# Kernel tuning notes

Measured on AMD Instinct MI355X. Metric: run time of the kernel, lower is better.

Reference implementation:

```python
import jax, jax.numpy as jnp
import numpy as np

N = 512
D = 128        # d_model
DE = 128       # d_edge
DFF = 2048
H = 8          # n_head
DH = D // H
LN_EPS = 1e-5


def layer_norm(x, g, b):
    m = jnp.mean(x, axis=-1, keepdims=True)
    v = jnp.mean((x - m) ** 2, axis=-1, keepdims=True)
    return (x - m) * jax.lax.rsqrt(v + LN_EPS) * g + b


def setup_inputs() -> dict:
    key = jax.random.key(0)
    ks = jax.random.split(key, 20)
    s = 0.02
    d = {
        "node": jax.random.normal(ks[0], (N, D), jnp.float32),
        "edge": jax.random.normal(ks[1], (N, N, DE), jnp.float32),
        "edge_mask": jnp.zeros((N, N), dtype=bool),
        # proj_memory: Linear(d_edge+2*d_model -> d_model) split by concat blocks [edge|src|tar]
        "w_mem_e": s * jax.random.normal(ks[2], (DE, D), jnp.float32),
        "w_mem_s": s * jax.random.normal(ks[3], (D, D), jnp.float32),
        "w_mem_t": s * jax.random.normal(ks[4], (D, D), jnp.float32),
        "b_mem": jnp.zeros((D,), jnp.float32),
        "g_ln_mem": jnp.ones((D,), jnp.float32),
        "b_ln_mem": jnp.zeros((D,), jnp.float32),
        # proj_edge: Linear(d_model -> d_edge) + LN, then norm_edge
        "w_pe": s * jax.random.normal(ks[5], (D, DE), jnp.float32),
        "b_pe": jnp.zeros((DE,), jnp.float32),
        "g_ln_pe": jnp.ones((DE,), jnp.float32),
        "b_ln_pe": jnp.zeros((DE,), jnp.float32),
        "g_ln_edge": jnp.ones((DE,), jnp.float32),
        "b_ln_edge": jnp.zeros((DE,), jnp.float32),
        # MHA in/out projections
        "wq": s * jax.random.normal(ks[6], (D, D), jnp.float32),
        "bq": jnp.zeros((D,), jnp.float32),
        "wk": s * jax.random.normal(ks[7], (D, D), jnp.float32),
        "bk": jnp.zeros((D,), jnp.float32),
        "wv": s * jax.random.normal(ks[8], (D, D), jnp.float32),
        "bv": jnp.zeros((D,), jnp.float32),
        "wo": s * jax.random.normal(ks[9], (D, D), jnp.float32),
        "bo": jnp.zeros((D,), jnp.float32),
        "g_ln2": jnp.ones((D,), jnp.float32),
        "b_ln2": jnp.zeros((D,), jnp.float32),
        # FFN
        "w_ff1": s * jax.random.normal(ks[10], (D, DFF), jnp.float32),
        "b_ff1": jnp.zeros((DFF,), jnp.float32),
        "w_ff2": s * jax.random.normal(ks[11], (DFF, D), jnp.float32),
        "b_ff2": jnp.zeros((D,), jnp.float32),
        "g_ln3": jnp.ones((D,), jnp.float32),
        "b_ln3": jnp.zeros((D,), jnp.float32),
    }
    return d


def reference(node, edge, edge_mask,
              w_mem_e, w_mem_s, w_mem_t, b_mem, g_ln_mem, b_ln_mem,
              w_pe, b_pe, g_ln_pe, b_ln_pe, g_ln_edge, b_ln_edge,
              wq, bq, wk, bk, wv, bv, wo, bo, g_ln2, b_ln2,
              w_ff1, b_ff1, w_ff2, b_ff2, g_ln3, b_ln3):
    # ---- _build_memory ----
    # torch concat order [edge, src_x, tar_x]: src_x[i,j]=node[j], tar_x[i,j]=node[i].
    # Avoid materializing the (N,N,2D+DE) concat: split the linear by block.
    mem_pre = (jnp.einsum('ijd,df->ijf', edge, w_mem_e)
               + (node @ w_mem_s)[None, :, :]
               + (node @ w_mem_t)[:, None, :]
               + b_mem)                                   # (N, N, D)
    memory = jax.nn.relu(layer_norm(mem_pre, g_ln_mem, b_ln_mem))
    edge_upd = jax.nn.relu(layer_norm(memory @ w_pe + b_pe, g_ln_pe, b_ln_pe))
    edge_new = layer_norm(edge + edge_upd, g_ln_edge, b_ln_edge)  # (N, N, DE)

    # ---- MHA: query len 1, batch N, key/value = memory (src_len=N, batch=N) ----
    q = (node @ wq + bq).reshape(N, H, DH)                # (Nb, H, DH)
    k = (jnp.einsum('snd,df->snf', memory, wk) + bk).reshape(N, N, H, DH)  # (S, Nb, H, DH)
    v = (jnp.einsum('snd,df->snf', memory, wv) + bv).reshape(N, N, H, DH)
    scores = jnp.einsum('nhd,snhd->nhs', q, k) / jnp.sqrt(jnp.float32(DH))  # (Nb, H, S)
    scores = jnp.where(edge_mask[:, None, :], jnp.finfo(scores.dtype).min, scores)
    attn = jax.nn.softmax(scores, axis=-1)
    ctx = jnp.einsum('nhs,snhd->nhd', attn, v).reshape(N, D)
    x_prime = ctx @ wo + bo                               # (N, D)

    # ---- residual + norms + FFN ----
    x = layer_norm(node + x_prime, g_ln2, b_ln2)
    ff = jax.nn.relu(x @ w_ff1 + b_ff1) @ w_ff2 + b_ff2
    x = layer_norm(x + ff, g_ln3, b_ln3)
    return (x, edge_new)
```

## Files before the change

### kernel.cpp

```cpp
#include <hip/hip_runtime.h>

#define NN 512
#define DD 128
#define DFF 2048
#define HH 8
#define DHH 16

typedef __attribute__((ext_vector_type(8))) short short8;
typedef __attribute__((ext_vector_type(4))) float f32x4;

static __device__ __forceinline__ float bf2f(ushort u) {
    union { unsigned int i; float f; } v; v.i = ((unsigned int)u) << 16; return v.f;
}
static __device__ __forceinline__ ushort f2bf(float f) {
    union { float f; unsigned int i; } v; v.f = f;
    unsigned int x = v.i;
    return (ushort)((x + 0x7fffu + ((x >> 16) & 1u)) >> 16);
}
static __device__ __forceinline__ short8 pack8(float4 v0, float4 v1) {
    short8 u;
    u[0]=(short)f2bf(v0.x); u[1]=(short)f2bf(v0.y);
    u[2]=(short)f2bf(v0.z); u[3]=(short)f2bf(v0.w);
    u[4]=(short)f2bf(v1.x); u[5]=(short)f2bf(v1.y);
    u[6]=(short)f2bf(v1.z); u[7]=(short)f2bf(v1.w);
    return u;
}

static __device__ __forceinline__ int probe_f32(const void* p) {
    return (((const ushort*)p)[0] == 0) ? 1 : 0;
}
static __device__ __forceinline__ float ld(const void* p, size_t i, int f32) {
    return f32 ? ((const float*)p)[i] : bf2f(((const ushort*)p)[i]);
}
static __device__ __forceinline__ void st(void* p, size_t i, float v, int f32) {
    if (f32) ((float*)p)[i] = v; else ((ushort*)p)[i] = f2bf(v);
}

static __device__ __forceinline__ ushort* mem_row_ptr(void* out_base, void* wsmem,
                                                      int big, int f32, int r) {
    if (big) return (ushort*)wsmem + (size_t)r * DD;
    char* b = (char*)out_base;
    return f32 ? (ushort*)(b + (size_t)4*NN*DD + (size_t)r*4*DD)
               : (ushort*)(b + (size_t)2*NN*DD + (size_t)r*2*DD);
}

static __device__ __forceinline__ int swz(int row, int b) {
    return row*256 + (b ^ ((row & 15) << 4));
}

static __device__ __forceinline__ float2 ln_tree(float v, float* red, float* red2) {
    const int t = threadIdx.x;
    __syncthreads();
    red[t] = v; red2[t] = v * v;
    __syncthreads();
    for (int s = 64; s > 0; s >>= 1) {
        if (t < s) { red[t] += red[t + s]; red2[t] += red2[t + s]; }
        __syncthreads();
    }
    float mean = red[0] * (1.f / 128.f);
    float var  = red2[0] * (1.f / 128.f) - mean * mean;
    float2 r; r.x = mean; r.y = rsqrtf(fmaxf(var, 0.f) + 1e-5f);
    return r;
}

__global__ __launch_bounds__(256) void k_wconv(
    const void* __restrict__ w_mem_e, const void* __restrict__ w_pe,
    const void* __restrict__ dt_probe, ushort* __restrict__ wf)
{
    const int f32 = probe_f32(dt_probe);
    int idx = blockIdx.x * 256 + threadIdx.x;
    const void* W = (idx < 32768) ? w_mem_e : w_pe;
    int rem = idx & 32767;
    int b = rem & 7, lane = (rem >> 3) & 63, ks = (rem >> 9) & 3, tn = rem >> 11;
    int k = ks*32 + (lane >> 4)*8 + b;
    int n = tn*16 + (lane & 15);
    wf[idx] = f2bf(ld(W, (size_t)k*DD + n, f32));
}

__global__ __launch_bounds__(256) void k_wconv2(
    const void* __restrict__ w_ff1, const void* __restrict__ w_ff2,
    const void* __restrict__ dt_probe, ushort* __restrict__ wf)
{
    const int f32 = probe_f32(dt_probe);
    int idx = blockIdx.x * 256 + threadIdx.x;
    if (idx < 262144) {
        int b = idx & 7, lane = (idx >> 3) & 63, ks = (idx >> 9) & 3, ct = idx >> 11;
        int k = ks*32 + (lane >> 4)*8 + b;
        int n = ct*16 + (lane & 15);
        wf[idx] = f2bf(ld(w_ff1, (size_t)k*DFF + n, f32));
    } else {
        int rem = idx - 262144;
        int b = rem & 7, lane = (rem >> 3) & 63, kc = (rem >> 9) & 63, tn = rem >> 15;
        int k = kc*32 + (lane >> 4)*8 + b;
        int n = tn*16 + (lane & 15);
        wf[idx] = f2bf(ld(w_ff2, (size_t)k*DD + n, f32));
    }
}

__global__ __launch_bounds__(128) void k_pre(
    const void* __restrict__ node, const void* __restrict__ w_mem_s,
    const void* __restrict__ w_mem_t, const void* __restrict__ wq,
    const void* __restrict__ bq, const void* __restrict__ wk,
    const void* __restrict__ bk, const void* __restrict__ dt_probe,
    float* __restrict__ a_s, float* __restrict__ a_t,
    float* __restrict__ qw, float* __restrict__ qb)
{
    const int f32 = probe_f32(dt_probe);
    const int n = blockIdx.x;
    const int t = threadIdx.x;
    __shared__ float nr[DD];
    __shared__ float qr[DD];
    nr[t] = ld(node, (size_t)n*DD + t, f32);
    __syncthreads();
    float s_acc = 0.f, t_acc = 0.f, q_acc = ld(bq, t, f32);
    for (int k = 0; k < DD; ++k) {
        float nv = nr[k];
        s_acc += nv * ld(w_mem_s, (size_t)k*DD + t, f32);
        t_acc += nv * ld(w_mem_t, (size_t)k*DD + t, f32);
        q_acc += nv * ld(wq,      (size_t)k*DD + t, f32);
    }
    a_s[(size_t)n*DD + t] = s_acc;
    a_t[(size_t)n*DD + t] = t_acc;
    qr[t] = q_acc;
    __syncthreads();
    for (int h = 0; h < HH; ++h) {
        float acc = 0.f;
        #pragma unroll
        for (int dh = 0; dh < DHH; ++dh)
            acc += qr[h*DHH + dh] * ld(wk, (size_t)t*DD + h*DHH + dh, f32);
        qw[((size_t)n*HH + h)*DD + t] = acc;
    }
    if (t < HH) {
        float acc = 0.f;
        #pragma unroll
        for (int dh = 0; dh < DHH; ++dh)
            acc += qr[t*DHH + dh] * ld(bk, (size_t)t*DHH + dh, f32);
        qb[(size_t)n*HH + t] = acc;
    }
}

__global__ __launch_bounds__(256) void k_fused(
    const void* __restrict__ edge, const ushort* __restrict__ wfe,
    const ushort* __restrict__ wfp, const void* __restrict__ b_mem,
    const void* __restrict__ g1, const void* __restrict__ b1,
    const void* __restrict__ b_pe, const void* __restrict__ g2,
    const void* __restrict__ b2, const void* __restrict__ g3,
    const void* __restrict__ b3, const void* __restrict__ dt_probe,
    const float* __restrict__ a_s, const float* __restrict__ a_t,
    void* __restrict__ out_base, ushort* __restrict__ memws)
{
    const int f32 = probe_f32(dt_probe);
    const int t = threadIdx.x;
    const int r0 = blockIdx.x * 64;
    const int i0 = r0 >> 9;
    const int j0 = r0 & (NN - 1);

    __shared__ __align__(16) ushort tile[64*128];

    const int lane = t & 63, w = t >> 6;
    const int rowbase = w * 16;
    const int l15 = lane & 15, g = lane >> 4;
    const int arow = r0 + rowbase + l15;

    short8 afr[4];
    if (f32) {
        const float* ep = (const float*)edge + (size_t)arow*DD;
        #pragma unroll
        for (int ks = 0; ks < 4; ++ks) {
            float4 v0 = *(const float4*)(ep + ks*32 + g*8);
            float4 v1 = *(const float4*)(ep + ks*32 + g*8 + 4);
            afr[ks] = pack8(v0, v1);
        }
    } else {
        const ushort* ep = (const ushort*)edge + (size_t)arow*DD;
        #pragma unroll
        for (int ks = 0; ks < 4; ++ks)
            afr[ks] = *(const short8*)(ep + ks*32 + g*8);
    }

    f32x4 acc[8];
    #pragma unroll
    for (int tn = 0; tn < 8; ++tn) {
        acc[tn][0]=0.f; acc[tn][1]=0.f; acc[tn][2]=0.f; acc[tn][3]=0.f;
    }
    #pragma unroll
    for (int tn = 0; tn < 8; ++tn) {
        #pragma unroll
        for (int ks = 0; ks < 4; ++ks) {
            short8 bfr = *(const short8*)(wfe + ((tn*4 + ks)*64 + lane)*8);
            acc[tn] = __builtin_amdgcn_mfma_f32_16x16x32_bf16(afr[ks], bfr,
                                                              acc[tn], 0, 0, 0);
        }
    }

    float atb[8], gg[8], bb[8];
    #pragma unroll
    for (int tn = 0; tn < 8; ++tn) {
        int c = tn*16 + l15;
        atb[tn] = a_t[(size_t)i0*DD + c] + ld(b_mem, c, f32);
        gg[tn]  = ld(g1, c, f32);
        bb[tn]  = ld(b1, c, f32);
    }

    float sum[4], sq[4];
    #pragma unroll
    for (int reg = 0; reg < 4; ++reg) {
        const int rr = rowbase + 4*g + reg;
        float s = 0.f, qq = 0.f;
        #pragma unroll
        for (int tn = 0; tn < 8; ++tn) {
            float v = acc[tn][reg]
                    + a_s[(size_t)(j0 + rr)*DD + tn*16 + l15] + atb[tn];
            acc[tn][reg] = v;
            s += v; qq += v*v;
        }
        sum[reg] = s; sq[reg] = qq;
    }
    #pragma unroll
    for (int m = 1; m < 16; m <<= 1) {
        #pragma unroll
        for (int reg = 0; reg < 4; ++reg) {
            sum[reg] += __shfl_xor(sum[reg], m, 64);
            sq[reg]  += __shfl_xor(sq[reg],  m, 64);
        }
    }
    #pragma unroll
    for (int reg = 0; reg < 4; ++reg) {
        const int rr = rowbase + 4*g + reg;
        float mean = sum[reg] * (1.f/128.f);
        float var  = sq[reg] * (1.f/128.f) - mean*mean;
        float rstd = rsqrtf(fmaxf(var, 0.f) + 1e-5f);
        #pragma unroll
        for (int tn = 0; tn < 8; ++tn) {
            float v = fmaxf((acc[tn][reg]-mean)*rstd*gg[tn] + bb[tn], 0.f);
            *(ushort*)((char*)tile + swz(rr, (tn*16 + l15)*2)) = f2bf(v);
        }
    }

    {
        const int crow = rowbase + l15;
        ushort* dst = memws + (size_t)(r0 + crow)*DD;
        #pragma unroll
        for (int q = 0; q < 4; ++q)
            *(short8*)(dst + g*32 + q*8) =
                *(const short8*)((const char*)tile + swz(crow, g*64 + q*16));
    }

    short8 afr2[4];
    #pragma unroll
    for (int ks = 0; ks < 4; ++ks)
        afr2[ks] = *(const short8*)((const char*)tile
                    + swz(rowbase + l15, ks*64 + g*16));

    f32x4 acc2[8];
    #pragma unroll
    for (int tn = 0; tn < 8; ++tn) {
        acc2[tn][0]=0.f; acc2[tn][1]=0.f; acc2[tn][2]=0.f; acc2[tn][3]=0.f;
    }
    #pragma unroll
    for (int tn = 0; tn < 8; ++tn) {
        #pragma unroll
        for (int ks = 0; ks < 4; ++ks) {
            short8 bfr = *(const short8*)(wfp + ((tn*4 + ks)*64 + lane)*8);
            acc2[tn] = __builtin_amdgcn_mfma_f32_16x16x32_bf16(afr2[ks], bfr,
                                                               acc2[tn], 0, 0, 0);
        }
    }

    float bpe[8], gg2[8], bb2[8], gg3v[8], bb3v[8];
    #pragma unroll
    for (int tn = 0; tn < 8; ++tn) {
        int c = tn*16 + l15;
        bpe[tn]  = ld(b_pe, c, f32);
        gg2[tn]  = ld(g2, c, f32); bb2[tn] = ld(b2, c, f32);
        gg3v[tn] = ld(g3, c, f32); bb3v[tn] = ld(b3, c, f32);
    }

    float s1[4], q1[4];
    #pragma unroll
    for (int reg = 0; reg < 4; ++reg) {
        float s = 0.f, qq = 0.f;
        #pragma unroll
        for (int tn = 0; tn < 8; ++tn) {
            float v = acc2[tn][reg] + bpe[tn];
            acc2[tn][reg] = v;
            s += v; qq += v*v;
        }
        s1[reg] = s; q1[reg] = qq;
    }
    #pragma unroll
    for (int m = 1; m < 16; m <<= 1) {
        #pragma unroll
        for (int reg = 0; reg < 4; ++reg) {
            s1[reg] += __shfl_xor(s1[reg], m, 64);
            q1[reg] += __shfl_xor(q1[reg], m, 64);
        }
    }

    float s2[4], q2[4];
    #pragma unroll
    for (int reg = 0; reg < 4; ++reg) {
        const int rr = rowbase + 4*g + reg;
        float mean = s1[reg] * (1.f/128.f);
        float var  = q1[reg] * (1.f/128.f) - mean*mean;
        float rstd = rsqrtf(fmaxf(var, 0.f) + 1e-5f);
        float ss = 0.f, qq = 0.f;
        #pragma unroll
        for (int tn = 0; tn < 8; ++tn) {
            float upd = fmaxf((acc2[tn][reg]-mean)*rstd*gg2[tn] + bb2[tn], 0.f);
            float ev  = ld(edge, (size_t)(r0 + rr)*DD + tn*16 + l15, f32);
            float y = ev + upd;
            acc2[tn][reg] = y;
            ss += y; qq += y*y;
        }
        s2[reg] = ss; q2[reg] = qq;
    }
    #pragma unroll
    for (int m = 1; m < 16; m <<= 1) {
        #pragma unroll
        for (int reg = 0; reg < 4; ++reg) {
            s2[reg] += __shfl_xor(s2[reg], m, 64);
            q2[reg] += __shfl_xor(q2[reg], m, 64);
        }
    }
    #pragma unroll
    for (int reg = 0; reg < 4; ++reg) {
        const int rr = rowbase + 4*g + reg;
        float mean = s2[reg] * (1.f/128.f);
        float var  = q2[reg] * (1.f/128.f) - mean*mean;
        float rstd = rsqrtf(fmaxf(var, 0.f) + 1e-5f);
        #pragma unroll
        for (int tn = 0; tn < 8; ++tn) {
            float outv = (acc2[tn][reg]-mean)*rstd*gg3v[tn] + bb3v[tn];
            st(out_base, (size_t)NN*DD + (size_t)(r0 + rr)*DD + tn*16 + l15,
               outv, f32);
        }
    }
}

__global__ __launch_bounds__(256) void k_mem_mfma(
    const void* __restrict__ edge, const ushort* __restrict__ wfe,
    const void* __restrict__ b_mem, const void* __restrict__ g1,
    const void* __restrict__ b1, const void* __restrict__ dt_probe,
    const float* __restrict__ a_s, const float* __restrict__ a_t,
    void* __restrict__ out_base, void* __restrict__ wsmem, int big)
{
    const int f32 = probe_f32(dt_probe);
    const int t = threadIdx.x;
    const int r0 = blockIdx.x * 64;
    const int i0 = r0 >> 9;
    const int j0 = r0 & (NN - 1);

    __shared__ __align__(16) ushort tile[64*128];

    {
        const int row = t >> 2;
        const int c0  = (t & 3) * 32;
        if (f32) {
            const float4* gp = (const float4*)((const float*)edge
                               + (size_t)(r0 + row)*DD + c0);
            #pragma unroll
            for (int q = 0; q < 4; ++q)
                *(short8*)((char*)tile + swz(row, c0*2 + q*16)) =
                    pack8(gp[2*q], gp[2*q+1]);
        } else {
            const short8* gp = (const short8*)((const ushort*)edge
                               + (size_t)(r0 + row)*DD + c0);
            #pragma unroll
            for (int q = 0; q < 4; ++q)
                *(short8*)((char*)tile + swz(row, c0*2 + q*16)) = gp[q];
        }
    }
    __syncthreads();

    const int lane = t & 63, w = t >> 6;
    const int rowbase = w * 16;
    const int l15 = lane & 15, g = lane >> 4;

    short8 afr[4];
    #pragma unroll
    for (int ks = 0; ks < 4; ++ks)
        afr[ks] = *(const short8*)((const char*)tile
                   + swz(rowbase + l15, ks*64 + g*16));

    f32x4 acc[8];
    #pragma unroll
    for (int tn = 0; tn < 8; ++tn) {
        acc[tn][0]=0.f; acc[tn][1]=0.f; acc[tn][2]=0.f; acc[tn][3]=0.f;
    }
    #pragma unroll
    for (int tn = 0; tn < 8; ++tn) {
        #pragma unroll
        for (int ks = 0; ks < 4; ++ks) {
            short8 bfr = *(const short8*)(wfe + ((tn*4 + ks)*64 + lane)*8);
            acc[tn] = __builtin_amdgcn_mfma_f32_16x16x32_bf16(afr[ks], bfr,
                                                              acc[tn], 0, 0, 0);
        }
    }

    float atb[8], gg[8], bb[8];
    #pragma unroll
    for (int tn = 0; tn < 8; ++tn) {
        int c = tn*16 + l15;
        atb[tn] = a_t[(size_t)i0*DD + c] + ld(b_mem, c, f32);
        gg[tn]  = ld(g1, c, f32);
        bb[tn]  = ld(b1, c, f32);
    }

    float sum[4], sq[4];
    #pragma unroll
    for (int reg = 0; reg < 4; ++reg) {
        const int rr = rowbase + 4*g + reg;
        float s = 0.f, qq = 0.f;
        #pragma unroll
        for (int tn = 0; tn < 8; ++tn) {
            float v = acc[tn][reg]
                    + a_s[(size_t)(j0 + rr)*DD + tn*16 + l15] + atb[tn];
            acc[tn][reg] = v;
            s += v; qq += v*v;
        }
        sum[reg] = s; sq[reg] = qq;
    }
    #pragma unroll
    for (int m = 1; m < 16; m <<= 1) {
        #pragma unroll
        for (int reg = 0; reg < 4; ++reg) {
            sum[reg] += __shfl_xor(sum[reg], m, 64);
            sq[reg]  += __shfl_xor(sq[reg],  m, 64);
        }
    }
    #pragma unroll
    for (int reg = 0; reg < 4; ++reg) {
        const int rr = rowbase + 4*g + reg;
        float mean = sum[reg] * (1.f/128.f);
        float var  = sq[reg] * (1.f/128.f) - mean*mean;
        float rstd = rsqrtf(fmaxf(var, 0.f) + 1e-5f);
        #pragma unroll
        for (int tn = 0; tn < 8; ++tn) {
            float v = fmaxf((acc[tn][reg]-mean)*rstd*gg[tn] + bb[tn], 0.f);
            *(ushort*)((char*)tile + swz(rr, (tn*16 + l15)*2)) = f2bf(v);
        }
    }
    __syncthreads();

    {
        const int crow = rowbase + l15;
        ushort* dst = mem_row_ptr(out_base, wsmem, big, f32, r0 + crow);
        #pragma unroll
        for (int q = 0; q < 4; ++q)
            *(short8*)(dst + g*32 + q*8) =
                *(const short8*)((const char*)tile + swz(crow, g*64 + q*16));
    }
}

__global__ __launch_bounds__(256) void k_attn(
    const float* __restrict__ qw, const float* __restrict__ qb,
    const unsigned char* __restrict__ mask,
    const void* __restrict__ wv_w, const void* __restrict__ bv,
    const void* __restrict__ dt_probe,
    void* __restrict__ out_base, void* __restrict__ wsmem, int big,
    float* __restrict__ ctx)
{
    const int f32 = probe_f32(dt_probe);
    const int n = blockIdx.x;
    const int t = threadIdx.x;

    __shared__ __align__(16) float qwl[HH*DD];
    __shared__ float qbl[HH];
    __shared__ __align__(16) float sc[HH*NN];
    __shared__ __align__(16) float msub[64*132];
    __shared__ float srd[HH*33];
    __shared__ __align__(16) float pml[HH*DD];

    #pragma unroll
    for (int u = 0; u < 4; ++u) qwl[t + 256*u] = qw[(size_t)n*HH*DD + t + 256*u];
    if (t < HH) qbl[t] = qb[(size_t)n*HH + t];
    __syncthreads();

    const int h0 = t >> 6;
    const int sl = t & 63;

    for (int s0 = 0; s0 < NN; s0 += 64) {
        __syncthreads();
        #pragma unroll
        for (int u = 0; u < 4; ++u) {
            int c = u*256 + t;
            int row = c >> 4, sub = c & 15;
            const ushort* src = mem_row_ptr(out_base, wsmem, big, f32,
                                            (s0 + row)*NN + n) + sub*8;
            short8 uv = *(const short8*)src;
            float4 x0, x1;
            x0.x=bf2f((ushort)uv[0]); x0.y=bf2f((ushort)uv[1]);
            x0.z=bf2f((ushort)uv[2]); x0.w=bf2f((ushort)uv[3]);
            x1.x=bf2f((ushort)uv[4]); x1.y=bf2f((ushort)uv[5]);
            x1.z=bf2f((ushort)uv[6]); x1.w=bf2f((ushort)uv[7]);
            float* d = msub + row*132 + sub*8;
            *(float4*)d = x0; *(float4*)(d + 4) = x1;
        }
        __syncthreads();
        float a0 = 0.f, a1 = 0.f;
        const float* mrow = msub + sl*132;
        const float* q0p = qwl + h0*DD;
        const float* q1p = qwl + (h0+4)*DD;
        for (int d = 0; d < DD; d += 4) {
            float4 mv = *(const float4*)(mrow + d);
            float4 qa = *(const float4*)(q0p + d);
            float4 qc = *(const float4*)(q1p + d);
            a0 += mv.x*qa.x + mv.y*qa.y + mv.z*qa.z + mv.w*qa.w;
            a1 += mv.x*qc.x + mv.y*qc.y + mv.z*qc.z + mv.w*qc.w;
        }
        int s = s0 + sl;
        int mk = mask[(size_t)n*NN + s] != 0;
        sc[h0*NN + s]     = mk ? -1.0e30f : 0.25f*(a0 + qbl[h0]);
        sc[(h0+4)*NN + s] = mk ? -1.0e30f : 0.25f*(a1 + qbl[h0+4]);
    }
    __syncthreads();

    {
        const int h = t >> 5, l = t & 31;
        float mx = -1.0e30f;
        for (int k = 0; k < 16; ++k) mx = fmaxf(mx, sc[h*NN + l + 32*k]);
        srd[h*33 + l] = mx;
        __syncthreads();
        for (int s = 16; s > 0; s >>= 1) {
            if (l < s) srd[h*33 + l] = fmaxf(srd[h*33 + l], srd[h*33 + l + s]);
            __syncthreads();
        }
        mx = srd[h*33];
        __syncthreads();
        float sum = 0.f;
        for (int k = 0; k < 16; ++k) {
            float e = __expf(sc[h*NN + l + 32*k] - mx);
            sc[h*NN + l + 32*k] = e;
            sum += e;
        }
        srd[h*33 + l] = sum;
        __syncthreads();
        for (int s = 16; s > 0; s >>= 1) {
            if (l < s) srd[h*33 + l] += srd[h*33 + l + s];
            __syncthreads();
        }
        float inv = 1.f / srd[h*33];
        for (int k = 0; k < 16; ++k) sc[h*NN + l + 32*k] *= inv;
    }
    __syncthreads();

    const int h2 = t >> 5, d4 = (t & 31) * 4;
    float4 acc2; acc2.x = 0.f; acc2.y = 0.f; acc2.z = 0.f; acc2.w = 0.f;
    for (int s0 = 0; s0 < NN; s0 += 64) {
        __syncthreads();
        #pragma unroll
        for (int u = 0; u < 4; ++u) {
            int c = u*256 + t;
            int row = c >> 4, sub = c & 15;
            const ushort* src = mem_row_ptr(out_base, wsmem, big, f32,
                                            (s0 + row)*NN + n) + sub*8;
            short8 uv = *(const short8*)src;
            float4 x0, x1;
            x0.x=bf2f((ushort)uv[0]); x0.y=bf2f((ushort)uv[1]);
            x0.z=bf2f((ushort)uv[2]); x0.w=bf2f((ushort)uv[3]);
            x1.x=bf2f((ushort)uv[4]); x1.y=bf2f((ushort)uv[5]);
            x1.z=bf2f((ushort)uv[6]); x1.w=bf2f((ushort)uv[7]);
            float* d = msub + row*132 + sub*8;
            *(float4*)d = x0; *(float4*)(d + 4) = x1;
        }
        __syncthreads();
        for (int s = 0; s < 64; ++s) {
            float wgt = sc[h2*NN + s0 + s];
            float4 mv = *(const float4*)(msub + s*132 + d4);
            acc2.x += wgt*mv.x; acc2.y += wgt*mv.y;
            acc2.z += wgt*mv.z; acc2.w += wgt*mv.w;
        }
    }
    *(float4*)(pml + h2*DD + d4) = acc2;
    __syncthreads();

    if (t < DD) {
        int h = t >> 4;
        float c = ld(bv, t, f32);
        const float* pr = pml + h*DD;
        for (int d = 0; d < DD; ++d)
            c += pr[d] * ld(wv_w, (size_t)d*DD + t, f32);
        ctx[(size_t)n*DD + t] = c;
    }
}

__global__ __launch_bounds__(256) void k_edge_mfma(
    const void* __restrict__ edge, const ushort* __restrict__ wfp,
    const void* __restrict__ b_pe, const void* __restrict__ g2,
    const void* __restrict__ b2, const void* __restrict__ g3,
    const void* __restrict__ b3, const void* __restrict__ dt_probe,
    void* __restrict__ out_base, void* __restrict__ wsmem, int big)
{
    const int f32 = probe_f32(dt_probe);
    const int t = threadIdx.x;
    const int r0 = blockIdx.x * 64;

    __shared__ __align__(16) ushort tile[64*128];
    __shared__ __align__(16) float  etile[64*132];

    {
        const int row = t >> 2, ch = t & 3;
        const ushort* src = mem_row_ptr(out_base, wsmem, big, f32, r0 + row);
        #pragma unroll
        for (int q = 0; q < 4; ++q) {
            short8 u = *(const short8*)(src + ch*32 + q*8);
            *(short8*)((char*)tile + swz(row, ch*64 + q*16)) = u;
        }
        float* ed = etile + row*132 + ch*32;
        if (f32) {
            const float4* gp = (const float4*)((const float*)edge
                               + (size_t)(r0 + row)*DD + ch*32);
            #pragma unroll
            for (int q = 0; q < 8; ++q) ((float4*)ed)[q] = gp[q];
        } else {
            const ushort* gp = (const ushort*)edge + (size_t)(r0 + row)*DD + ch*32;
            #pragma unroll
            for (int q = 0; q < 4; ++q) {
                short8 u = *(const short8*)(gp + q*8);
                float4 x0, x1;
                x0.x=bf2f((ushort)u[0]); x0.y=bf2f((ushort)u[1]);
                x0.z=bf2f((ushort)u[2]); x0.w=bf2f((ushort)u[3]);
                x1.x=bf2f((ushort)u[4]); x1.y=bf2f((ushort)u[5]);
                x1.z=bf2f((ushort)u[6]); x1.w=bf2f((ushort)u[7]);
                ((float4*)ed)[2*q] = x0; ((float4*)ed)[2*q+1] = x1;
            }
        }
    }
    __syncthreads();

    const int lane = t & 63, w = t >> 6;
    const int rowbase = w * 16;
    const int l15 = lane & 15, g = lane >> 4;

    short8 afr[4];
    #pragma unroll
    for (int ks = 0; ks < 4; ++ks)
        afr[ks] = *(const short8*)((const char*)tile
                   + swz(rowbase + l15, ks*64 + g*16));

    f32x4 acc[8];
    #pragma unroll
    for (int tn = 0; tn < 8; ++tn) {
        acc[tn][0]=0.f; acc[tn][1]=0.f; acc[tn][2]=0.f; acc[tn][3]=0.f;
    }
    #pragma unroll
    for (int tn = 0; tn < 8; ++tn) {
        #pragma unroll
        for (int ks = 0; ks < 4; ++ks) {
            short8 bfr = *(const short8*)(wfp + ((tn*4 + ks)*64 + lane)*8);
            acc[tn] = __builtin_amdgcn_mfma_f32_16x16x32_bf16(afr[ks], bfr,
                                                              acc[tn], 0, 0, 0);
        }
    }

    float bpe[8], gg2[8], bb2[8], gg3[8], bb3[8];
    #pragma unroll
    for (int tn = 0; tn < 8; ++tn) {
        int c = tn*16 + l15;
        bpe[tn] = ld(b_pe, c, f32);
        gg2[tn] = ld(g2, c, f32); bb2[tn] = ld(b2, c, f32);
        gg3[tn] = ld(g3, c, f32); bb3[tn] = ld(b3, c, f32);
    }

    float sum[4], sq[4];
    #pragma unroll
    for (int reg = 0; reg < 4; ++reg) {
        float s = 0.f, qq = 0.f;
        #pragma unroll
        for (int tn = 0; tn < 8; ++tn) {
            float v = acc[tn][reg] + bpe[tn];
            acc[tn][reg] = v;
            s += v; qq += v*v;
        }
        sum[reg] = s; sq[reg] = qq;
    }
    #pragma unroll
    for (int m = 1; m < 16; m <<= 1) {
        #pragma unroll
        for (int reg = 0; reg < 4; ++reg) {
            sum[reg] += __shfl_xor(sum[reg], m, 64);
            sq[reg]  += __shfl_xor(sq[reg],  m, 64);
        }
    }

    float sum2[4], sq2[4];
    #pragma unroll
    for (int reg = 0; reg < 4; ++reg) {
        const int rr = rowbase + 4*g + reg;
        float mean = sum[reg] * (1.f/128.f);
        float var  = sq[reg] * (1.f/128.f) - mean*mean;
        float rstd = rsqrtf(fmaxf(var, 0.f) + 1e-5f);
        float s2 = 0.f, q2 = 0.f;
        #pragma unroll
        for (int tn = 0; tn < 8; ++tn) {
            float upd = fmaxf((acc[tn][reg]-mean)*rstd*gg2[tn] + bb2[tn], 0.f);
            float y = etile[rr*132 + tn*16 + l15] + upd;
            acc[tn][reg] = y;
            s2 += y; q2 += y*y;
        }
        sum2[reg] = s2; sq2[reg] = q2;
    }
    #pragma unroll
    for (int m = 1; m < 16; m <<= 1) {
        #pragma unroll
        for (int reg = 0; reg < 4; ++reg) {
            sum2[reg] += __shfl_xor(sum2[reg], m, 64);
            sq2[reg]  += __shfl_xor(sq2[reg],  m, 64);
        }
    }
    #pragma unroll
    for (int reg = 0; reg < 4; ++reg) {
        const int rr = rowbase + 4*g + reg;
        float mean = sum2[reg] * (1.f/128.f);
        float var  = sq2[reg] * (1.f/128.f) - mean*mean;
        float rstd = rsqrtf(fmaxf(var, 0.f) + 1e-5f);
        #pragma unroll
        for (int tn = 0; tn < 8; ++tn)
            etile[rr*132 + tn*16 + l15] =
                (acc[tn][reg]-mean)*rstd*gg3[tn] + bb3[tn];
    }
    __syncthreads();

    {
        const int crow = rowbase + l15;
        const size_t rbase = (size_t)NN*DD + (size_t)(r0 + crow)*DD + g*32;
        const float* srcl = etile + crow*132 + g*32;
        if (f32) {
            float* dst = (float*)out_base + rbase;
            #pragma unroll
            for (int q = 0; q < 8; ++q)
                *(float4*)(dst + q*4) = *(const float4*)(srcl + q*4);
        } else {
            ushort* dst = (ushort*)out_base + rbase;
            #pragma unroll
            for (int q = 0; q < 4; ++q) {
                float4 v0 = *(const float4*)(srcl + q*8);
                float4 v1 = *(const float4*)(srcl + q*8 + 4);
                *(short8*)(dst + q*8) = pack8(v0, v1);
            }
        }
    }
}

__global__ __launch_bounds__(128) void k_post1(
    const float* __restrict__ ctx, const void* __restrict__ wo,
    const void* __restrict__ bo, const void* __restrict__ node,
    const void* __restrict__ g2, const void* __restrict__ b2,
    const void* __restrict__ dt_probe, float* __restrict__ xbuf,
    float* __restrict__ out_acc)
{
    const int f32 = probe_f32(dt_probe);
    const int n = blockIdx.x;
    const int t = threadIdx.x;
    __shared__ float cr[DD];
    __shared__ float red[DD], red2[DD];

    out_acc[(size_t)n*DD + t] = 0.f;

    cr[t] = ctx[(size_t)n*DD + t];
    __syncthreads();
    float xp = ld(bo, t, f32);
    for (int k = 0; k < DD; ++k)
        xp += cr[k] * ld(wo, (size_t)k*DD + t, f32);
    float x0 = ld(node, (size_t)n*DD + t, f32) + xp;
    float2 st1 = ln_tree(x0, red, red2);
    xbuf[(size_t)n*DD + t] = (x0 - st1.x) * st1.y * ld(g2, t, f32) + ld(b2, t, f32);
}

__global__ __launch_bounds__(256) void k_ffn_sk(
    const float* __restrict__ xbuf, const ushort* __restrict__ wf1,
    const ushort* __restrict__ wf2, const void* __restrict__ b1,
    const void* __restrict__ dt_probe, float* __restrict__ out_acc)
{
    const int f32 = probe_f32(dt_probe);
    const int t = threadIdx.x;
    const int rt = blockIdx.x & 7;
    const int kt = blockIdx.x >> 3;
    const int r0 = rt * 64;

    __shared__ __align__(16) ushort xt[64*128];
    __shared__ __align__(16) ushort ht[64*128];

    {
        const int row = t >> 2, c0 = (t & 3) * 32;
        const float4* gp = (const float4*)(xbuf + (size_t)(r0 + row)*DD + c0);
        #pragma unroll
        for (int q = 0; q < 4; ++q)
            *(short8*)((char*)xt + swz(row, c0*2 + q*16)) =
                pack8(gp[2*q], gp[2*q+1]);
    }
    __syncthreads();

    const int lane = t & 63, w = t >> 6;
    const int rowbase = w * 16;
    const int l15 = lane & 15, g = lane >> 4;

    short8 afr[4];
    #pragma unroll
    for (int ks = 0; ks < 4; ++ks)
        afr[ks] = *(const short8*)((const char*)xt
                   + swz(rowbase + l15, ks*64 + g*16));

    f32x4 hacc[8];
    #pragma unroll
    for (int tn = 0; tn < 8; ++tn) {
        hacc[tn][0]=0.f; hacc[tn][1]=0.f; hacc[tn][2]=0.f; hacc[tn][3]=0.f;
    }
    #pragma unroll
    for (int tn = 0; tn < 8; ++tn) {
        #pragma unroll
        for (int ks = 0; ks < 4; ++ks) {
            short8 bfr = *(const short8*)(wf1
                          + (((size_t)(kt*8 + tn)*4 + ks)*64 + lane)*8);
            hacc[tn] = __builtin_amdgcn_mfma_f32_16x16x32_bf16(afr[ks], bfr,
                                                               hacc[tn], 0, 0, 0);
        }
    }
    float b1v[8];
    #pragma unroll
    for (int tn = 0; tn < 8; ++tn)
        b1v[tn] = ld(b1, kt*128 + tn*16 + l15, f32);
    #pragma unroll
    for (int reg = 0; reg < 4; ++reg) {
        const int rr = rowbase + 4*g + reg;
        #pragma unroll
        for (int tn = 0; tn < 8; ++tn) {
            float v = fmaxf(hacc[tn][reg] + b1v[tn], 0.f);
            *(ushort*)((char*)ht + swz(rr, (tn*16 + l15)*2)) = f2bf(v);
        }
    }
    __syncthreads();

    short8 afr2[4];
    #pragma unroll
    for (int ks = 0; ks < 4; ++ks)
        afr2[ks] = *(const short8*)((const char*)ht
                    + swz(rowbase + l15, ks*64 + g*16));
    f32x4 oacc[8];
    #pragma unroll
    for (int tn = 0; tn < 8; ++tn) {
        oacc[tn][0]=0.f; oacc[tn][1]=0.f; oacc[tn][2]=0.f; oacc[tn][3]=0.f;
    }
    #pragma unroll
    for (int tn = 0; tn < 8; ++tn) {
        #pragma unroll
        for (int ks = 0; ks < 4; ++ks) {
            short8 bfr = *(const short8*)(wf2
                          + (((size_t)tn*64 + kt*4 + ks)*64 + lane)*8);
            oacc[tn] = __builtin_amdgcn_mfma_f32_16x16x32_bf16(afr2[ks], bfr,
                                                               oacc[tn], 0, 0, 0);
        }
    }

    #pragma unroll
    for (int reg = 0; reg < 4; ++reg) {
        const int rr = rowbase + 4*g + reg;
        #pragma unroll
        for (int tn = 0; tn < 8; ++tn)
            unsafeAtomicAdd(&out_acc[(size_t)(r0 + rr)*DD + tn*16 + l15],
                            oacc[tn][reg]);
    }
}

__global__ __launch_bounds__(128) void k_ffn_fin(
    const float* __restrict__ xbuf, const float* __restrict__ out_acc,
    const void* __restrict__ b2f, const void* __restrict__ g3,
    const void* __restrict__ b3, const void* __restrict__ dt_probe,
    void* __restrict__ out_base)
{
    const int f32 = probe_f32(dt_probe);
    const int n = blockIdx.x;
    const int t = threadIdx.x;
    __shared__ float red[DD], red2[DD];

    float y = xbuf[(size_t)n*DD + t] + out_acc[(size_t)n*DD + t]
            + ld(b2f, t, f32);
    float2 st2 = ln_tree(y, red, red2);
    float outv = (y - st2.x) * st2.y * ld(g3, t, f32) + ld(b3, t, f32);
    st(out_base, (size_t)n*DD + t, outv, f32);
}

extern "C" void kernel_launch(void* const* d_in, const int* in_sizes, int n_in,
                              void* d_out, int out_size, void* d_ws, size_t ws_size,
                              hipStream_t stream)
{
    const void* node     = d_in[0];
    const void* edge     = d_in[1];
    const unsigned char* mask = (const unsigned char*)d_in[2];
    const void* w_mem_e  = d_in[3];
    const void* w_mem_s  = d_in[4];
    const void* w_mem_t  = d_in[5];
    const void* b_mem    = d_in[6];
    const void* g_ln_mem = d_in[7];
    const void* b_ln_mem = d_in[8];
    const void* w_pe     = d_in[9];
    const void* b_pe     = d_in[10];
    const void* g_ln_pe  = d_in[11];
    const void* b_ln_pe  = d_in[12];
    const void* g_ln_edge= d_in[13];
    const void* b_ln_edge= d_in[14];
    const void* wq       = d_in[15];
    const void* bq       = d_in[16];
    const void* wk       = d_in[17];
    const void* bk       = d_in[18];
    const void* wv       = d_in[19];
    const void* bv       = d_in[20];
    const void* wo       = d_in[21];
    const void* bo       = d_in[22];
    const void* g_ln2    = d_in[23];
    const void* b_ln2    = d_in[24];
    const void* w_ff1    = d_in[25];
    const void* b_ff1    = d_in[26];
    const void* w_ff2    = d_in[27];
    const void* b_ff2    = d_in[28];
    const void* g_ln3    = d_in[29];
    const void* b_ln3    = d_in[30];

    float* wsf  = (float*)d_ws;
    float* a_s  = wsf;
    float* a_t  = wsf +  65536;
    float* qw   = wsf + 131072;
    float* qb   = wsf + 655360;
    float* ctxp = wsf + 659456;
    ushort* wf1 = (ushort*)d_ws;
    ushort* wf2 = (ushort*)d_ws + 262144;
    float* xbuf = wsf + 262144;
    float* oaccp= wsf + 327680;
    void*  wsmem = (char*)d_ws + (size_t)4*1024*1024;
    int big = (ws_size >= (size_t)72*1024*1024) ? 1 : 0;

    const void* probe = g_ln_mem;

    ushort* wfe = (ushort*)d_out;
    ushort* wfp = wfe + 32768;

    k_wconv<<<256, 256, 0, stream>>>(w_mem_e, w_pe, probe, wfe);
    k_pre<<<NN, 128, 0, stream>>>(node, w_mem_s, w_mem_t, wq, bq, wk, bk, probe,
                                  a_s, a_t, qw, qb);
    if (big) {
        k_fused<<<(NN*NN)/64, 256, 0, stream>>>(edge, wfe, wfp, b_mem,
                                                g_ln_mem, b_ln_mem, b_pe,
                                                g_ln_pe, b_ln_pe, g_ln_edge,
                                                b_ln_edge, probe, a_s, a_t,
                                                d_out, (ushort*)wsmem);
        k_attn<<<NN, 256, 0, stream>>>(qw, qb, mask, wv, bv, probe,
                                       d_out, wsmem, 1, ctxp);
        k_wconv2<<<2048, 256, 0, stream>>>(w_ff1, w_ff2, probe, wf1);
    } else {
        k_mem_mfma<<<(NN*NN)/64, 256, 0, stream>>>(edge, wfe, b_mem, g_ln_mem,
                                                   b_ln_mem, probe, a_s, a_t,
                                                   d_out, wsmem, big);
        k_attn<<<NN, 256, 0, stream>>>(qw, qb, mask, wv, bv, probe,
                                       d_out, wsmem, big, ctxp);
        k_wconv2<<<2048, 256, 0, stream>>>(w_ff1, w_ff2, probe, wf1);
        k_edge_mfma<<<(NN*NN)/64, 256, 0, stream>>>(edge, wfp, b_pe, g_ln_pe,
                                                    b_ln_pe, g_ln_edge,
                                                    b_ln_edge, probe, d_out,
                                                    wsmem, big);
    }
    k_post1<<<NN, 128, 0, stream>>>(ctxp, wo, bo, node, g_ln2, b_ln2,
                                    probe, xbuf, oaccp);
    k_ffn_sk<<<128, 256, 0, stream>>>(xbuf, wf1, wf2, b_ff1, probe, oaccp);
    k_ffn_fin<<<NN, 128, 0, stream>>>(xbuf, oaccp, b_ff2, g_ln3, b_ln3,
                                      probe, d_out);
}
```

Before: 552.1 us.

## Transpose memory workspace and stage whole per-node tile in LDS for attention

The memory workspace is now written in transposed order (target-major), so each attention block reads its 512x128 bf16 slice as one contiguous stream instead of strided rows. The attention kernel loads that whole slice once into a swizzled 128KB LDS tile and reuses it for both the score pass and the weighted-sum pass. Before, the same data was fetched from global memory twice, in 64-row chunks. The cost is a large LDS footprint that limits each CU to one 256-thread block, leaving little latency hiding. Scores are now computed per row for all 8 heads from bf16 data unpacked on the fly.

```diff
diff --git a/kernel.cpp b/kernel.cpp
--- a/kernel.cpp
+++ b/kernel.cpp
@@ -239,7 +239,7 @@
 
     {
         const int crow = rowbase + l15;
-        ushort* dst = memws + (size_t)(r0 + crow)*DD;
+        ushort* dst = memws + ((size_t)(j0 + crow)*NN + i0)*DD;
         #pragma unroll
         for (int q = 0; q < 4; ++q)
             *(short8*)(dst + g*32 + q*8) =
@@ -465,54 +465,53 @@
     const int n = blockIdx.x;
     const int t = threadIdx.x;
 
+    __shared__ __align__(16) ushort mtile[NN*DD];
+    __shared__ __align__(16) float sc[HH*NN];
     __shared__ __align__(16) float qwl[HH*DD];
     __shared__ float qbl[HH];
-    __shared__ __align__(16) float sc[HH*NN];
-    __shared__ __align__(16) float msub[64*132];
     __shared__ float srd[HH*33];
     __shared__ __align__(16) float pml[HH*DD];
 
     #pragma unroll
     for (int u = 0; u < 4; ++u) qwl[t + 256*u] = qw[(size_t)n*HH*DD + t + 256*u];
     if (t < HH) qbl[t] = qb[(size_t)n*HH + t];
-    __syncthreads();
-
-    const int h0 = t >> 6;
-    const int sl = t & 63;
-
-    for (int s0 = 0; s0 < NN; s0 += 64) {
-        __syncthreads();
-        #pragma unroll
-        for (int u = 0; u < 4; ++u) {
-            int c = u*256 + t;
-            int row = c >> 4, sub = c & 15;
-            const ushort* src = mem_row_ptr(out_base, wsmem, big, f32,
-                                            (s0 + row)*NN + n) + sub*8;
-            short8 uv = *(const short8*)src;
-            float4 x0, x1;
-            x0.x=bf2f((ushort)uv[0]); x0.y=bf2f((ushort)uv[1]);
-            x0.z=bf2f((ushort)uv[2]); x0.w=bf2f((ushort)uv[3]);
-            x1.x=bf2f((ushort)uv[4]); x1.y=bf2f((ushort)uv[5]);
-            x1.z=bf2f((ushort)uv[6]); x1.w=bf2f((ushort)uv[7]);
-            float* d = msub + row*132 + sub*8;
-            *(float4*)d = x0; *(float4*)(d + 4) = x1;
-        }
-        __syncthreads();
-        float a0 = 0.f, a1 = 0.f;
-        const float* mrow = msub + sl*132;
-        const float* q0p = qwl + h0*DD;
-        const float* q1p = qwl + (h0+4)*DD;
-        for (int d = 0; d < DD; d += 4) {
-            float4 mv = *(const float4*)(mrow + d);
-            float4 qa = *(const float4*)(q0p + d);
-            float4 qc = *(const float4*)(q1p + d);
-            a0 += mv.x*qa.x + mv.y*qa.y + mv.z*qa.z + mv.w*qa.w;
-            a1 += mv.x*qc.x + mv.y*qc.y + mv.z*qc.z + mv.w*qc.w;
-        }
-        int s = s0 + sl;
+
+    const ushort* base_big = (const ushort*)wsmem + (size_t)n*NN*DD;
+    for (int u = 0; u < 32; ++u) {
+        int idx = u*256 + t;
+        int row = idx >> 4, q = idx & 15;
+        short8 v;
+        if (big) v = *(const short8*)(base_big + (size_t)idx*8);
+        else     v = *(const short8*)(mem_row_ptr(out_base, wsmem, 0, f32,
+                                                  row*NN + n) + q*8);
+        *(short8*)((char*)mtile + row*256 + ((q ^ (row & 15)) << 4)) = v;
+    }
+    __syncthreads();
+
+    #pragma unroll
+    for (int r = 0; r < 2; ++r) {
+        int s = t + 256*r;
+        float acc[8];
+        #pragma unroll
+        for (int h = 0; h < 8; ++h) acc[h] = 0.f;
+        const char* rowp = (const char*)mtile + s*256;
+        const int sx = (s & 15) << 4;
+        #pragma unroll 4
+        for (int q = 0; q < 16; ++q) {
+            short8 uv = *(const short8*)(rowp + ((q << 4) ^ sx));
+            #pragma unroll
+            for (int e = 0; e < 8; ++e) {
+                float xv = bf2f((ushort)uv[e]);
+                const float* qc = qwl + q*8 + e;
+                #pragma unroll
+                for (int h = 0; h < 8; ++h)
+                    acc[h] += xv * qc[h*DD];
+            }
+        }
         int mk = mask[(size_t)n*NN + s] != 0;
-        sc[h0*NN + s]     = mk ? -1.0e30f : 0.25f*(a0 + qbl[h0]);
-        sc[(h0+4)*NN + s] = mk ? -1.0e30f : 0.25f*(a1 + qbl[h0+4]);
+        #pragma unroll
+        for (int h = 0; h < 8; ++h)
+            sc[h*NN + s] = mk ? -1.0e30f : 0.25f*(acc[h] + qbl[h]);
     }
     __syncthreads();
 
@@ -545,34 +544,21 @@
     }
     __syncthreads();
 
-    const int h2 = t >> 5, d4 = (t & 31) * 4;
-    float4 acc2; acc2.x = 0.f; acc2.y = 0.f; acc2.z = 0.f; acc2.w = 0.f;
-    for (int s0 = 0; s0 < NN; s0 += 64) {
-        __syncthreads();
-        #pragma unroll
-        for (int u = 0; u < 4; ++u) {
-            int c = u*256 + t;
-            int row = c >> 4, sub = c & 15;
-            const ushort* src = mem_row_ptr(out_base, wsmem, big, f32,
-                                            (s0 + row)*NN + n) + sub*8;
-            short8 uv = *(const short8*)src;
-            float4 x0, x1;
-            x0.x=bf2f((ushort)uv[0]); x0.y=bf2f((ushort)uv[1]);
-            x0.z=bf2f((ushort)uv[2]); x0.w=bf2f((ushort)uv[3]);
-            x1.x=bf2f((ushort)uv[4]); x1.y=bf2f((ushort)uv[5]);
-            x1.z=bf2f((ushort)uv[6]); x1.w=bf2f((ushort)uv[7]);
-            float* d = msub + row*132 + sub*8;
-            *(float4*)d = x0; *(float4*)(d + 4) = x1;
-        }
-        __syncthreads();
-        for (int s = 0; s < 64; ++s) {
-            float wgt = sc[h2*NN + s0 + s];
-            float4 mv = *(const float4*)(msub + s*132 + d4);
-            acc2.x += wgt*mv.x; acc2.y += wgt*mv.y;
-            acc2.z += wgt*mv.z; acc2.w += wgt*mv.w;
-        }
-    }
-    *(float4*)(pml + h2*DD + d4) = acc2;
+    {
+        const int h2 = t >> 5, l31 = t & 31;
+        const int q2 = l31 >> 1, o2 = (l31 & 1) * 8;
+        float4 acc2; acc2.x = 0.f; acc2.y = 0.f; acc2.z = 0.f; acc2.w = 0.f;
+        for (int s = 0; s < NN; ++s) {
+            float wgt = sc[h2*NN + s];
+            const ushort* mv = (const ushort*)((const char*)mtile + s*256
+                                + (((q2 ^ (s & 15)) << 4) + o2));
+            acc2.x += wgt * bf2f(mv[0]);
+            acc2.y += wgt * bf2f(mv[1]);
+            acc2.z += wgt * bf2f(mv[2]);
+            acc2.w += wgt * bf2f(mv[3]);
+        }
+        *(float4*)(pml + h2*DD + l31*4) = acc2;
+    }
     __syncthreads();
 
     if (t < DD) {
```

After: 561.3 us. No clear change (+1.7%).
